# Optimization experiments

Hardware: AMD Instinct MI355X
Metric: run time of the kernel (lower is better)

## Reference

```python
import jax, jax.numpy as jnp
import numpy as np

N = 100000   # nodes
D = 128      # feature dim
E = 1600000  # edges (avg degree 16)
BN_EPS = 1e-5


def setup_inputs() -> dict:
    key = jax.random.key(0)
    ks = jax.random.split(key, 8)
    x = jax.random.normal(ks[0], (N, D), dtype=jnp.float32)
    edge_index = jax.random.randint(ks[1], (2, E), 0, N, dtype=jnp.int64)
    W = jax.random.normal(ks[2], (D, D), dtype=jnp.float32) * 0.05   # GCNConv linear weight
    b = jax.random.normal(ks[3], (D,), dtype=jnp.float32) * 0.05     # GCNConv bias
    gamma = jax.random.uniform(ks[4], (D,), dtype=jnp.float32) + 0.5 # BN weight
    beta = jax.random.normal(ks[5], (D,), dtype=jnp.float32) * 0.1   # BN bias
    running_mean = jax.random.normal(ks[6], (D,), dtype=jnp.float32) * 0.1
    running_var = jax.random.uniform(ks[7], (D,), dtype=jnp.float32) + 0.5
    return {"x": x, "edge_index": edge_index, "W": W, "b": b,
            "gamma": gamma, "beta": beta,
            "running_mean": running_mean, "running_var": running_var}


def reference(x, edge_index, W, b, gamma, beta, running_mean, running_var):
    # --- GCNConv (default: add self-loops, symmetric normalization) ---
    h = x @ W                                        # [N, D]
    loops = jnp.arange(N, dtype=edge_index.dtype)
    src = jnp.concatenate([edge_index[0], loops])    # [E+N]
    dst = jnp.concatenate([edge_index[1], loops])    # [E+N]
    deg = jax.ops.segment_sum(jnp.ones_like(dst, dtype=h.dtype), dst, num_segments=N)
    dinv = jax.lax.rsqrt(jnp.maximum(deg, 1.0))      # deg >= 1 due to self-loops
    norm = dinv[src] * dinv[dst]                     # [E+N]
    agg = jax.ops.segment_sum(h[src] * norm[:, None], dst, num_segments=N)  # [N, D]
    agg = agg + b
    # --- BatchNorm1d (inference: running stats) ---
    bn = (agg - running_mean) * jax.lax.rsqrt(running_var + BN_EPS) * gamma + beta
    # --- ReLU + residual (dropout is identity in eval) ---
    return jax.nn.relu(bn) + x
```

## Files before the change

kernel.cpp:

```cpp
#include <hip/hip_runtime.h>

#define D 128
#define BN_EPS 1e-5f
#define NBUCK 512
#define BSHIFT 8
#define BNODES 256
#define CAP 4608

using short8 = __attribute__((ext_vector_type(8))) short;
using floatx4 = __attribute__((ext_vector_type(4))) float;

__device__ inline unsigned short f2bf(float f) {
    unsigned u = __float_as_uint(f);
    u += 0x7fff + ((u >> 16) & 1);
    return (unsigned short)(u >> 16);
}
__device__ inline float bf2f(unsigned short s) {
    return __uint_as_float(((unsigned)s) << 16);
}

__global__ __launch_bounds__(256) void init_kernel(
    const float* __restrict__ W, const float* __restrict__ b,
    const float* __restrict__ gamma, const float* __restrict__ beta,
    const float* __restrict__ mean, const float* __restrict__ var,
    unsigned short* __restrict__ Wt, float* __restrict__ scv,
    float* __restrict__ pov, int* __restrict__ resCnt) {
    int t = blockIdx.x * 256 + threadIdx.x;
    Wt[(size_t)(t & 127) * D + (t >> 7)] = f2bf(W[t]);
    if (t < NBUCK) resCnt[t] = 0;
    if (t < D) {
        float sc = gamma[t] * rsqrtf(var[t] + BN_EPS);
        scv[t] = sc;
        pov[t] = (b[t] - mean[t]) * sc + beta[t];
    }
}

__global__ __launch_bounds__(512) void pB_kernel(const int* __restrict__ src,
                                                 const int* __restrict__ dst,
                                                 int* __restrict__ resCnt,
                                                 unsigned int* __restrict__ pairs,
                                                 int E) {
    __shared__ int lh[NBUCK];
    __shared__ int lcur[NBUCK];
    int tid = threadIdx.x;
    lh[tid] = 0;
    __syncthreads();
    int chunk = (E + gridDim.x - 1) / gridDim.x;
    int base = blockIdx.x * chunk;
    int lim = min(chunk, E - base);
    if (lim <= 0) return;
    for (int i = tid; i < lim; i += 512) atomicAdd(&lh[dst[base + i] >> BSHIFT], 1);
    __syncthreads();
    int c = lh[tid];
    lcur[tid] = tid * CAP + (c ? atomicAdd(&resCnt[tid], c) : 0);
    __syncthreads();
    for (int i = tid; i < lim; i += 512) {
        int s = src[base + i], d2 = dst[base + i];
        int b2 = d2 >> BSHIFT;
        int pos = atomicAdd(&lcur[b2], 1);
        if (pos < (b2 + 1) * CAP)
            pairs[pos] = (((unsigned)d2 & 255u) << 24) | (unsigned)s;
    }
}

__global__ __launch_bounds__(512) void sortxs_kernel(
    const unsigned int* __restrict__ pairs, const int* __restrict__ resCnt,
    const int* __restrict__ src, const int* __restrict__ dst,
    const float* __restrict__ x, int* __restrict__ deg, int* __restrict__ offs,
    int* __restrict__ colidx, float* __restrict__ dinv,
    unsigned short* __restrict__ xs, int N, int E) {
    __shared__ int sb[NBUCK];
    __shared__ int lh[BNODES];
    __shared__ int lcur[BNODES];
    __shared__ float sdv[BNODES];
    int tid = threadIdx.x;
    int b = blockIdx.x;
    sb[tid] = resCnt[tid];
    __syncthreads();
    for (int d = 1; d < NBUCK; d <<= 1) {
        int v = (tid >= d) ? sb[tid - d] : 0;
        __syncthreads();
        sb[tid] += v;
        __syncthreads();
    }
    int cnt = resCnt[b];
    int cbase = sb[b] - cnt;
    int pbase = b * CAP;
    if (tid < BNODES) lh[tid] = 0;
    __syncthreads();

    if (cnt <= CAP) {
        for (int i = tid; i < cnt; i += 512)
            atomicAdd(&lh[pairs[pbase + i] >> 24], 1);
        __syncthreads();
        int orig = (tid < BNODES) ? lh[tid] : 0;
        for (int d = 1; d < BNODES; d <<= 1) {
            int v = (tid < BNODES && tid >= d) ? lh[tid - d] : 0;
            __syncthreads();
            if (tid < BNODES) lh[tid] += v;
            __syncthreads();
        }
        if (tid < BNODES) {
            int exc = lh[tid] - orig;
            int node = b * BNODES + tid;
            float dvv = rsqrtf((float)(orig + 1));
            sdv[tid] = dvv;
            if (node < N) {
                deg[node] = orig;
                offs[node] = cbase + exc;
                dinv[node] = dvv;
            }
            lcur[tid] = exc;
        }
        __syncthreads();
        for (int i = tid; i < cnt; i += 512) {
            unsigned int p = pairs[pbase + i];
            int pos = atomicAdd(&lcur[p >> 24], 1);
            colidx[cbase + pos] = (int)(p & 0x00FFFFFFu);
        }
    } else {
        for (int i = tid; i < E; i += 512) {
            int d2 = dst[i];
            if ((d2 >> BSHIFT) == b) atomicAdd(&lh[d2 & 255], 1);
        }
        __syncthreads();
        if (tid < BNODES) {
            int orig = lh[tid];
            int node = b * BNODES + tid;
            float dvv = rsqrtf((float)(orig + 1));
            sdv[tid] = dvv;
            if (node < N) {
                deg[node] = orig;
                offs[node] = -1;
                dinv[node] = dvv;
            }
        }
        __syncthreads();
    }

    int nb = min(BNODES, N - b * BNODES);
    if (nb > 0) {
        const float4* x4 = (const float4*)x;
        ushort4* xs4 = (ushort4*)xs;
        int tot = nb * 32;
        for (int c2 = tid; c2 < tot; c2 += 512) {
            int nl = c2 >> 5, q = c2 & 31;
            int node = b * BNODES + nl;
            float dvv = sdv[nl];
            float4 f = x4[(size_t)node * 32 + q];
            ushort4 o;
            o.x = f2bf(dvv * f.x); o.y = f2bf(dvv * f.y);
            o.z = f2bf(dvv * f.z); o.w = f2bf(dvv * f.w);
            xs4[(size_t)node * 32 + q] = o;
        }
    }
}

__global__ __launch_bounds__(1024, 8) void aggemm_kernel(
    const unsigned short* __restrict__ xs, const float* __restrict__ dinv,
    const int* __restrict__ offs, const int* __restrict__ deg,
    const int* __restrict__ colidx, const int* __restrict__ src,
    const int* __restrict__ dst, const float* __restrict__ xg,
    const unsigned short* __restrict__ Wt, const float* __restrict__ scv,
    const float* __restrict__ pov, float* __restrict__ outp, int N, int E) {
    __shared__ unsigned int sA[16][68];
    int tid = threadIdx.x;
    int lane = tid & 63;
    int w = tid >> 6;
    int row0 = blockIdx.x * 16;
    int node = row0 + w;
    const unsigned int* xs32 = (const unsigned int*)xs;

    if (node < N) {
        float dv = dinv[node];
        unsigned int sv = xs32[(size_t)node * 64 + lane];
        float a0 = bf2f((unsigned short)sv);
        float a1 = bf2f((unsigned short)(sv >> 16));
        int p = offs[node];
        if (p >= 0) {
            int pe = p + deg[node];
            for (; p + 16 <= pe; p += 16) {
                int u[16];
                unsigned int v[16];
#pragma unroll
                for (int j = 0; j < 16; ++j) u[j] = colidx[p + j];
#pragma unroll
                for (int j = 0; j < 16; ++j) v[j] = xs32[(size_t)u[j] * 64 + lane];
#pragma unroll
                for (int j = 0; j < 16; ++j) {
                    a0 += bf2f((unsigned short)v[j]);
                    a1 += bf2f((unsigned short)(v[j] >> 16));
                }
            }
            for (; p + 4 <= pe; p += 4) {
                int u[4];
                unsigned int v[4];
#pragma unroll
                for (int j = 0; j < 4; ++j) u[j] = colidx[p + j];
#pragma unroll
                for (int j = 0; j < 4; ++j) v[j] = xs32[(size_t)u[j] * 64 + lane];
#pragma unroll
                for (int j = 0; j < 4; ++j) {
                    a0 += bf2f((unsigned short)v[j]);
                    a1 += bf2f((unsigned short)(v[j] >> 16));
                }
            }
            for (; p < pe; ++p) {
                unsigned int v = xs32[(size_t)colidx[p] * 64 + lane];
                a0 += bf2f((unsigned short)v);
                a1 += bf2f((unsigned short)(v >> 16));
            }
        } else {
            for (int e = 0; e < E; ++e) {
                if (dst[e] == node) {
                    unsigned int v = xs32[(size_t)src[e] * 64 + lane];
                    a0 += bf2f((unsigned short)v);
                    a1 += bf2f((unsigned short)(v >> 16));
                }
            }
        }
        sA[w][lane] =
            (unsigned int)f2bf(dv * a0) | ((unsigned int)f2bf(dv * a1) << 16);
    } else {
        sA[w][lane] = 0u;
    }
    __syncthreads();

    if (w < 8) {
        int m = lane & 15, quad = lane >> 4;
        short8 B[4];
#pragma unroll
        for (int ks = 0; ks < 4; ++ks)
            B[ks] = *(const short8*)&Wt[(size_t)(w * 16 + m) * D + ks * 32 + quad * 8];
        short8 A[4];
#pragma unroll
        for (int ks = 0; ks < 4; ++ks)
            A[ks] = *(const short8*)&sA[m][ks * 16 + quad * 4];
        floatx4 acc = {0.f, 0.f, 0.f, 0.f};
#pragma unroll
        for (int ks = 0; ks < 4; ++ks)
            acc = __builtin_amdgcn_mfma_f32_16x16x32_bf16(A[ks], B[ks], acc, 0, 0, 0);
        int col = w * 16 + m;
        float sc = scv[col], po = pov[col];
#pragma unroll
        for (int i = 0; i < 4; ++i) {
            int row = row0 + quad * 4 + i;
            if (row < N) {
                float bn = acc[i] * sc + po;
                size_t idx = (size_t)row * D + col;
                outp[idx] = fmaxf(bn, 0.f) + xg[idx];
            }
        }
    }
}

__global__ void wt_kernel(const float* __restrict__ W, const float* __restrict__ b,
                          const float* __restrict__ gamma, const float* __restrict__ beta,
                          const float* __restrict__ mean, const float* __restrict__ var,
                          unsigned short* __restrict__ Wt, float* __restrict__ scv,
                          float* __restrict__ pov) {
    int t = blockIdx.x * blockDim.x + threadIdx.x;
    int k = t >> 7, n = t & 127;
    Wt[(size_t)n * D + k] = f2bf(W[t]);
    if (t < D) {
        float sc = gamma[t] * rsqrtf(var[t] + BN_EPS);
        scv[t] = sc;
        pov[t] = (b[t] - mean[t]) * sc + beta[t];
    }
}

__global__ void deg_kernel(const int* __restrict__ dst, int* __restrict__ deg, int E) {
    int e = blockIdx.x * blockDim.x + threadIdx.x;
    if (e < E) atomicAdd(&deg[dst[e]], 1);
}

__global__ void dinv_kernel(const int* __restrict__ deg, float* __restrict__ dinv, int N) {
    int v = blockIdx.x * blockDim.x + threadIdx.x;
    if (v < N) dinv[v] = rsqrtf((float)(deg[v] + 1));
}

__global__ __launch_bounds__(256) void scan1_kernel(const int* __restrict__ deg,
                                                    int* __restrict__ bsum, int N) {
    __shared__ int s[256];
    int t = threadIdx.x;
    int v = blockIdx.x * 256 + t;
    s[t] = (v < N) ? deg[v] : 0;
    for (int st = 128; st > 0; st >>= 1) {
        __syncthreads();
        if (t < st) s[t] += s[t + st];
    }
    if (t == 0) bsum[blockIdx.x] = s[0];
}

__global__ __launch_bounds__(512) void scan2_kernel(int* __restrict__ bsum,
                                                    int* __restrict__ offs, int P, int N) {
    __shared__ int a[512];
    int t = threadIdx.x;
    int orig = (t < P) ? bsum[t] : 0;
    a[t] = orig;
    __syncthreads();
    for (int d = 1; d < 512; d <<= 1) {
        int tv = (t >= d) ? a[t - d] : 0;
        __syncthreads();
        a[t] += tv;
        __syncthreads();
    }
    if (t < P) bsum[t] = a[t] - orig;
    if (t == 0) offs[N] = a[511];
}

__global__ __launch_bounds__(256) void scan3_kernel(const int* __restrict__ deg,
                                                    const int* __restrict__ bsum,
                                                    int* __restrict__ offs,
                                                    int* __restrict__ cursor, int N) {
    __shared__ int a[256];
    int t = threadIdx.x;
    int v = blockIdx.x * 256 + t;
    int d = (v < N) ? deg[v] : 0;
    a[t] = d;
    __syncthreads();
    for (int st = 1; st < 256; st <<= 1) {
        int tv = (t >= st) ? a[t - st] : 0;
        __syncthreads();
        a[t] += tv;
        __syncthreads();
    }
    if (v < N) {
        int off = bsum[blockIdx.x] + a[t] - d;
        offs[v] = off;
        cursor[v] = off;
    }
}

__global__ void fill_kernel(const int* __restrict__ src, const int* __restrict__ dst,
                            int* __restrict__ cursor, int* __restrict__ colidx, int E) {
    int e = blockIdx.x * blockDim.x + threadIdx.x;
    if (e < E) {
        int d = dst[e];
        int pos = atomicAdd(&cursor[d], 1);
        colidx[pos] = src[e];
    }
}

__global__ __launch_bounds__(256) void agg_kernel(
    const float* __restrict__ x, const float* __restrict__ dinv,
    const int* __restrict__ offs, const int* __restrict__ deg,
    const int* __restrict__ colidx, float* __restrict__ outp, int N) {
    int wid = (blockIdx.x * blockDim.x + threadIdx.x) >> 6;
    if (wid >= N) return;
    int lane = threadIdx.x & 63;
    float dv = dinv[wid];
    int p = offs[wid];
    int pe = p + deg[wid];
    const float2* x2 = (const float2*)x;
    float2 s = x2[(size_t)wid * 64 + lane];
    float a0 = dv * s.x;
    float a1 = dv * s.y;
    for (; p < pe; ++p) {
        int u = colidx[p];
        float du = dinv[u];
        float2 vv = x2[(size_t)u * 64 + lane];
        a0 += du * vv.x;
        a1 += du * vv.y;
    }
    float2 r;
    r.x = dv * a0;
    r.y = dv * a1;
    ((float2*)outp)[(size_t)wid * 64 + lane] = r;
}

__global__ __launch_bounds__(256) void gemm_kernel(
    float* __restrict__ outp, const float* __restrict__ xg,
    const unsigned short* __restrict__ Wt, const float* __restrict__ scv,
    const float* __restrict__ pov, int nTiles) {
    __shared__ uint4 sW4[2048];
    int tid = threadIdx.x;
    const uint4* W4 = (const uint4*)Wt;
#pragma unroll
    for (int i = 0; i < 8; ++i) {
        int q = tid + i * 256;
        int row = q >> 4, c4 = q & 15;
        sW4[row * 16 + (c4 ^ (row & 7))] = W4[q];
    }
    __syncthreads();

    int wid = (blockIdx.x * blockDim.x + tid) >> 6;
    if (wid >= nTiles) return;
    int lane = tid & 63;
    int m = lane & 15, quad = lane >> 4;
    int row0 = wid * 16;

    short8 A[4];
    const float* arow = outp + (size_t)(row0 + m) * D;
#pragma unroll
    for (int ks = 0; ks < 4; ++ks) {
        float4 f0 = *(const float4*)(arow + ks * 32 + quad * 8);
        float4 f1 = *(const float4*)(arow + ks * 32 + quad * 8 + 4);
        short8 af;
        af[0] = (short)f2bf(f0.x); af[1] = (short)f2bf(f0.y);
        af[2] = (short)f2bf(f0.z); af[3] = (short)f2bf(f0.w);
        af[4] = (short)f2bf(f1.x); af[5] = (short)f2bf(f1.y);
        af[6] = (short)f2bf(f1.z); af[7] = (short)f2bf(f1.w);
        A[ks] = af;
    }

#pragma unroll
    for (int cg2 = 0; cg2 < 8; ++cg2) {
        int brow = cg2 * 16 + m;
        floatx4 acc = {0.f, 0.f, 0.f, 0.f};
#pragma unroll
        for (int ks = 0; ks < 4; ++ks) {
            short8 Bf = *(const short8*)&sW4[brow * 16 + ((ks * 4 + quad) ^ (m & 7))];
            acc = __builtin_amdgcn_mfma_f32_16x16x32_bf16(A[ks], Bf, acc, 0, 0, 0);
        }
        int col = cg2 * 16 + m;
        float sc = scv[col], po = pov[col];
#pragma unroll
        for (int i = 0; i < 4; ++i) {
            int row = row0 + quad * 4 + i;
            float bn = acc[i] * sc + po;
            size_t idx = (size_t)row * D + col;
            outp[idx] = fmaxf(bn, 0.f) + xg[idx];
        }
    }
}

extern "C" void kernel_launch(void* const* d_in, const int* in_sizes, int n_in,
                              void* d_out, int out_size, void* d_ws, size_t ws_size,
                              hipStream_t stream) {
    const float* x = (const float*)d_in[0];
    const int* edge = (const int*)d_in[1];
    const float* Wm = (const float*)d_in[2];
    const float* b = (const float*)d_in[3];
    const float* gamma = (const float*)d_in[4];
    const float* beta = (const float*)d_in[5];
    const float* mean = (const float*)d_in[6];
    const float* var = (const float*)d_in[7];
    float* out = (float*)d_out;

    int N = in_sizes[0] / D;
    int E = in_sizes[1] / 2;
    const int* src = edge;
    const int* dst = edge + E;
    int P = (N + 255) / 256;

    char* w = (char*)d_ws;
    size_t cur = 0;
    auto take = [&](size_t bytes) -> void* {
        cur = (cur + 15) & ~(size_t)15;
        void* p = w + cur;
        cur += bytes;
        return p;
    };
    int* deg = (int*)take((size_t)N * 4);
    int* resCnt = (int*)take(NBUCK * 4);
    float* dinv = (float*)take((size_t)N * 4);
    int* offs = (int*)take((size_t)(N + 1) * 4);
    int* cursor = (int*)take((size_t)N * 4);
    int* bsum = (int*)take((size_t)(P + 1) * 4);
    unsigned short* Wt = (unsigned short*)take((size_t)D * D * 2);
    float* scv = (float*)take(D * 4);
    float* pov = (float*)take(D * 4);
    int* colidx = (int*)take((size_t)E * 4);
    cur = (cur + 15) & ~(size_t)15;
    size_t fixedEnd = cur;

    size_t xsBytes = (size_t)N * D * 2;
    size_t pairsBytes = (size_t)NBUCK * CAP * 4;
    size_t zoneBytes = (xsBytes > pairsBytes) ? xsBytes : pairsBytes;
    bool fast = (fixedEnd + xsBytes + zoneBytes <= ws_size) && (N < (1 << 24));

    unsigned short* xs = nullptr;
    unsigned int* pairs = nullptr;
    if (fast) {
        xs = (unsigned short*)(w + fixedEnd);
        pairs = (unsigned int*)(w + fixedEnd + xsBytes);
    }

    if (fast) {
        init_kernel<<<(D * D) / 256, 256, 0, stream>>>(Wm, b, gamma, beta, mean, var,
                                                       Wt, scv, pov, resCnt);
        pB_kernel<<<128, 512, 0, stream>>>(src, dst, resCnt, pairs, E);
        sortxs_kernel<<<NBUCK, 512, 0, stream>>>(pairs, resCnt, src, dst, x, deg, offs,
                                                 colidx, dinv, xs, N, E);
        aggemm_kernel<<<(N + 15) / 16, 1024, 0, stream>>>(
            xs, dinv, offs, deg, colidx, src, dst, x, Wt, scv, pov, out, N, E);
    } else {
        wt_kernel<<<(D * D) / 256, 256, 0, stream>>>(Wm, b, gamma, beta, mean, var, Wt,
                                                     scv, pov);
        hipMemsetAsync(deg, 0, sizeof(int) * N, stream);
        deg_kernel<<<(E + 255) / 256, 256, 0, stream>>>(dst, deg, E);
        dinv_kernel<<<(N + 255) / 256, 256, 0, stream>>>(deg, dinv, N);
        scan1_kernel<<<P, 256, 0, stream>>>(deg, bsum, N);
        scan2_kernel<<<1, 512, 0, stream>>>(bsum, offs, P, N);
        scan3_kernel<<<P, 256, 0, stream>>>(deg, bsum, offs, cursor, N);
        fill_kernel<<<(E + 255) / 256, 256, 0, stream>>>(src, dst, cursor, colidx, E);
        agg_kernel<<<(N * 64 + 255) / 256, 256, 0, stream>>>(x, dinv, offs, deg, colidx,
                                                             out, N);
        int nTiles = (N + 15) / 16;
        gemm_kernel<<<(nTiles * 64 + 255) / 256, 256, 0, stream>>>(out, x, Wt, scv, pov,
                                                                   nTiles);
    }
}
```

Measured before the change: 281.4 us.

## Sort nodes by degree so each aggregation block handles similar workloads

Adds a degree histogram in the sort kernel and a new counting-sort kernel that builds a permutation of nodes grouped by in-degree. The fused aggregation+GEMM kernel then processes nodes in permuted order, so the 16 waves of a block have similar edge counts and less time is spent waiting on the slowest wave. The cost is an extra kernel launch, indirect reads of the permutation, and scattered output rows instead of contiguous ones.

After: 566.7 us. 2.01x slower.

```diff
diff --git a/kernel.cpp b/kernel.cpp
--- a/kernel.cpp
+++ b/kernel.cpp
@@ -24,10 +24,14 @@
     const float* __restrict__ gamma, const float* __restrict__ beta,
     const float* __restrict__ mean, const float* __restrict__ var,
     unsigned short* __restrict__ Wt, float* __restrict__ scv,
-    float* __restrict__ pov, int* __restrict__ resCnt) {
+    float* __restrict__ pov, int* __restrict__ resCnt,
+    int* __restrict__ dbins ,
+    int* __restrict__ perm, int N) {
     int t = blockIdx.x * 256 + threadIdx.x;
     Wt[(size_t)(t & 127) * D + (t >> 7)] = f2bf(W[t]);
     if (t < NBUCK) resCnt[t] = 0;
+    if (t < 256) dbins[t] = 0;
+    if (t < 16) perm[N + t] = N;
     if (t < D) {
         float sc = gamma[t] * rsqrtf(var[t] + BN_EPS);
         scv[t] = sc;
@@ -68,14 +72,16 @@
     const int* __restrict__ src, const int* __restrict__ dst,
     const float* __restrict__ x, int* __restrict__ deg, int* __restrict__ offs,
     int* __restrict__ colidx, float* __restrict__ dinv,
-    unsigned short* __restrict__ xs, int N, int E) {
+    unsigned short* __restrict__ xs, int* __restrict__ dcnt, int N, int E) {
     __shared__ int sb[NBUCK];
     __shared__ int lh[BNODES];
     __shared__ int lcur[BNODES];
     __shared__ float sdv[BNODES];
+    __shared__ int ldh[128];
     int tid = threadIdx.x;
     int b = blockIdx.x;
     sb[tid] = resCnt[tid];
+    if (tid < 128) ldh[tid] = 0;
     __syncthreads();
     for (int d = 1; d < NBUCK; d <<= 1) {
         int v = (tid >= d) ? sb[tid - d] : 0;
@@ -109,6 +115,7 @@
                 deg[node] = orig;
                 offs[node] = cbase + exc;
                 dinv[node] = dvv;
+                atomicAdd(&ldh[min(orig, 127)], 1);
             }
             lcur[tid] = exc;
         }
@@ -133,10 +140,12 @@
                 deg[node] = orig;
                 offs[node] = -1;
                 dinv[node] = dvv;
-            }
-        }
-        __syncthreads();
-    }
+                atomicAdd(&ldh[min(orig, 127)], 1);
+            }
+        }
+        __syncthreads();
+    }
+    if (tid < 128 && ldh[tid]) atomicAdd(&dcnt[tid], ldh[tid]);
 
     int nb = min(BNODES, N - b * BNODES);
     if (nb > 0) {
@@ -156,19 +165,45 @@
     }
 }
 
+__global__ __launch_bounds__(256) void dperm_kernel(
+    const int* __restrict__ deg, const int* __restrict__ dcnt,
+    int* __restrict__ dcur, int* __restrict__ perm, int N) {
+    __shared__ int inc[128];
+    __shared__ int exc[128];
+    int tid = threadIdx.x;
+    int orig = (tid < 128) ? dcnt[tid] : 0;
+    if (tid < 128) inc[tid] = orig;
+    __syncthreads();
+    for (int d = 1; d < 128; d <<= 1) {
+        int v = (tid < 128 && tid >= d) ? inc[tid - d] : 0;
+        __syncthreads();
+        if (tid < 128) inc[tid] += v;
+        __syncthreads();
+    }
+    if (tid < 128) exc[tid] = inc[tid] - orig;
+    __syncthreads();
+    int gsz = gridDim.x * 256;
+    for (int n = blockIdx.x * 256 + tid; n < N; n += gsz) {
+        int d = min(deg[n], 127);
+        int pos = exc[d] + atomicAdd(&dcur[d], 1);
+        perm[pos] = n;
+    }
+}
+
 __global__ __launch_bounds__(1024, 8) void aggemm_kernel(
     const unsigned short* __restrict__ xs, const float* __restrict__ dinv,
     const int* __restrict__ offs, const int* __restrict__ deg,
     const int* __restrict__ colidx, const int* __restrict__ src,
     const int* __restrict__ dst, const float* __restrict__ xg,
     const unsigned short* __restrict__ Wt, const float* __restrict__ scv,
-    const float* __restrict__ pov, float* __restrict__ outp, int N, int E) {
+    const float* __restrict__ pov, const int* __restrict__ perm,
+    float* __restrict__ outp, int N, int E) {
     __shared__ unsigned int sA[16][68];
     int tid = threadIdx.x;
     int lane = tid & 63;
     int w = tid >> 6;
     int row0 = blockIdx.x * 16;
-    int node = row0 + w;
+    int node = perm[row0 + w];
     const unsigned int* xs32 = (const unsigned int*)xs;
 
     if (node < N) {
@@ -244,10 +279,10 @@
         float sc = scv[col], po = pov[col];
 #pragma unroll
         for (int i = 0; i < 4; ++i) {
-            int row = row0 + quad * 4 + i;
-            if (row < N) {
+            int prow = perm[row0 + quad * 4 + i];
+            if (prow < N) {
                 float bn = acc[i] * sc + po;
-                size_t idx = (size_t)row * D + col;
+                size_t idx = (size_t)prow * D + col;
                 outp[idx] = fmaxf(bn, 0.f) + xg[idx];
             }
         }
@@ -456,7 +491,7 @@
     int* resCnt = (int*)take(NBUCK * 4);
     float* dinv = (float*)take((size_t)N * 4);
     int* offs = (int*)take((size_t)(N + 1) * 4);
-    int* cursor = (int*)take((size_t)N * 4);
+    int* cursor = (int*)take((size_t)(N + 16) * 4);
     int* bsum = (int*)take((size_t)(P + 1) * 4);
     unsigned short* Wt = (unsigned short*)take((size_t)D * D * 2);
     float* scv = (float*)take(D * 4);
@@ -468,7 +503,8 @@
     size_t xsBytes = (size_t)N * D * 2;
     size_t pairsBytes = (size_t)NBUCK * CAP * 4;
     size_t zoneBytes = (xsBytes > pairsBytes) ? xsBytes : pairsBytes;
-    bool fast = (fixedEnd + xsBytes + zoneBytes <= ws_size) && (N < (1 << 24));
+    bool fast = (fixedEnd + xsBytes + zoneBytes <= ws_size) && (N < (1 << 24)) &&
+                (P + 1 >= 256);
 
     unsigned short* xs = nullptr;
     unsigned int* pairs = nullptr;
@@ -478,13 +514,18 @@
     }
 
     if (fast) {
+        int* perm = cursor;
+        int* dcnt = bsum;
+        int* dcur = bsum + 128;
         init_kernel<<<(D * D) / 256, 256, 0, stream>>>(Wm, b, gamma, beta, mean, var,
-                                                       Wt, scv, pov, resCnt);
+                                                       Wt, scv, pov, resCnt, dcnt, perm,
+                                                       N);
         pB_kernel<<<128, 512, 0, stream>>>(src, dst, resCnt, pairs, E);
         sortxs_kernel<<<NBUCK, 512, 0, stream>>>(pairs, resCnt, src, dst, x, deg, offs,
-                                                 colidx, dinv, xs, N, E);
+                                                 colidx, dinv, xs, dcnt, N, E);
+        dperm_kernel<<<256, 256, 0, stream>>>(deg, dcnt, dcur, perm, N);
         aggemm_kernel<<<(N + 15) / 16, 1024, 0, stream>>>(
-            xs, dinv, offs, deg, colidx, src, dst, x, Wt, scv, pov, out, N, E);
+            xs, dinv, offs, deg, colidx, src, dst, x, Wt, scv, pov, perm, out, N, E);
     } else {
         wt_kernel<<<(D * D) / 256, 256, 0, stream>>>(Wm, b, gamma, beta, mean, var, Wt,
                                                      scv, pov);
```
